# Performance work log

Measured on AMD Instinct MI355X. Metric: run time of the kernel, lower is better.

Reference implementation:

```python
import jax, jax.numpy as jnp
import numpy as np

B, S, HID, NH, AH, F = 1024, 100, 128, 2, 64, 2
DH = HID // NH          # item/pos head size = 64
DA = AH // NH           # attribute head size = 32
EPS = 1e-12


def setup_inputs() -> dict:
    key = jax.random.key(0)
    ks = iter(jax.random.split(key, 32))
    n = lambda shape, s=0.02: jax.random.normal(next(ks), shape, dtype=jnp.float32) * s
    inp = {
        "input_tensor": jax.random.normal(next(ks), (B, S, HID), dtype=jnp.float32),
        "attribute_table": jax.random.normal(next(ks), (F, B, S, AH), dtype=jnp.float32),
        "position_embedding": jax.random.normal(next(ks), (B, S, HID), dtype=jnp.float32),
        "attention_mask": jnp.zeros((B, 1, S, S), dtype=jnp.float32),
        # item / positional projections (stored [in, out])
        "Wq": n((HID, HID)), "bq": jnp.zeros((HID,), jnp.float32),
        "Wk": n((HID, HID)), "bk": jnp.zeros((HID,), jnp.float32),
        "Wv": n((HID, HID)), "bv": jnp.zeros((HID,), jnp.float32),
        "Wqp": n((HID, HID)), "bqp": jnp.zeros((HID,), jnp.float32),
        "Wkp": n((HID, HID)), "bkp": jnp.zeros((HID,), jnp.float32),
        # per-attribute projections, stacked over feat axis
        "Wq_attr": n((F, AH, AH)), "bq_attr": jnp.zeros((F, AH), jnp.float32),
        "Wk_attr": n((F, AH, AH)), "bk_attr": jnp.zeros((F, AH), jnp.float32),
        # gate fusion (VanillaAttentionX): Linear(S,S) -> ReLU -> Linear(S,1)
        "fuse_W1": n((S, S)), "fuse_b1": jnp.zeros((S,), jnp.float32),
        "fuse_W2": n((S, 1)), "fuse_b2": jnp.zeros((1,), jnp.float32),
        # output dense + LayerNorm
        "Wd": n((HID, HID)), "bd": jnp.zeros((HID,), jnp.float32),
        "ln_g": jnp.ones((HID,), jnp.float32), "ln_b": jnp.zeros((HID,), jnp.float32),
    }
    return inp


def _split_heads(x, nh):  # [B,S,nh*d] -> [B,nh,S,d]
    b, s, hd = x.shape
    return x.reshape(b, s, nh, hd // nh).transpose(0, 2, 1, 3)


def reference(input_tensor, attribute_table, position_embedding, attention_mask,
              Wq, bq, Wk, bk, Wv, bv, Wqp, bqp, Wkp, bkp,
              Wq_attr, bq_attr, Wk_attr, bk_attr,
              fuse_W1, fuse_b1, fuse_W2, fuse_b2,
              Wd, bd, ln_g, ln_b):
    b, s, hid = input_tensor.shape
    # item / positional QKV
    q = _split_heads(input_tensor @ Wq + bq, NH)
    k = _split_heads(input_tensor @ Wk + bk, NH)
    v = _split_heads(input_tensor @ Wv + bv, NH)
    qp = _split_heads(position_embedding @ Wqp + bqp, NH)
    kp = _split_heads(position_embedding @ Wkp + bkp, NH)
    item_scores = jnp.einsum('bhqd,bhkd->bhqk', q, k)
    pos_scores = jnp.einsum('bhqd,bhkd->bhqk', qp, kp)
    # attribute score streams: [F,B,S,AH] -> [F,B,NH,S,DA]
    aq = jnp.einsum('fbsa,fao->fbso', attribute_table, Wq_attr) + bq_attr[:, None, None, :]
    ak = jnp.einsum('fbsa,fao->fbso', attribute_table, Wk_attr) + bk_attr[:, None, None, :]
    aq = aq.reshape(F, b, s, NH, DA).transpose(0, 1, 3, 2, 4)
    ak = ak.reshape(F, b, s, NH, DA).transpose(0, 1, 3, 2, 4)
    attr_scores = jnp.einsum('fbhqd,fbhkd->fbhqk', aq, ak)  # [F,B,NH,S,S]
    # gate fusion: stack streams on axis -2 -> [B,NH,S,F+2,S]
    stacked = jnp.concatenate([
        jnp.moveaxis(attr_scores, 0, 3),
        item_scores[:, :, :, None, :],
        pos_scores[:, :, :, None, :],
    ], axis=-2)
    energy = jax.nn.relu(stacked @ fuse_W1 + fuse_b1) @ fuse_W2 + fuse_b2  # [B,NH,S,F+2,1]
    gate_w = jax.nn.softmax(energy[..., 0], axis=-1)                       # [B,NH,S,F+2]
    fused = jnp.einsum('bhsfk,bhsf->bhsk', stacked, gate_w)                # [B,NH,S,S]
    scores = fused / jnp.sqrt(jnp.asarray(DH, fused.dtype)) + attention_mask
    probs = jax.nn.softmax(scores, axis=-1)
    ctx = jnp.einsum('bhqk,bhkd->bhqd', probs, v)
    ctx = ctx.transpose(0, 2, 1, 3).reshape(b, s, hid)
    h = ctx @ Wd + bd + input_tensor
    mu = jnp.mean(h, axis=-1, keepdims=True)
    var = jnp.mean((h - mu) ** 2, axis=-1, keepdims=True)
    return (h - mu) / jnp.sqrt(var + EPS) * ln_g + ln_b
```

## Files before the change

### kernel.cpp

```cpp
#include <hip/hip_runtime.h>
#include <hip/hip_bf16.h>

using bf16 = __hip_bfloat16;
using u16 = unsigned short;
typedef __attribute__((ext_vector_type(8))) short bf16x8;
typedef __attribute__((ext_vector_type(16))) float f32x16;

namespace {

constexpr int B_  = 1024;
constexpr int Sd  = 100;
constexpr int BS_ = B_ * Sd;

constexpr int NTHR = 1024;
constexpr int NW   = 16;

constexpr int STP = 420;
constexpr int STS = 104;
constexpr int QKP = 196;
constexpr int AP  = 132;
constexpr int ATP = 68;
constexpr int W1P = 116;
constexpr int VTP = 116;

constexpr int O_ST = 0;
constexpr int O_Q  = 84000;
constexpr int O_K  = 123200;
constexpr int E2S  = 32000;
constexpr int LBYTES = 162400;

constexpr int WQT_E  = 0;
constexpr int WKT_E  = 16384;
constexpr int WQPT_E = 32768;
constexpr int WKPT_E = 49152;
constexpr int WVT_E  = 65536;
constexpr int WAT_E  = 81920;
constexpr int W1T_E  = 98304;
constexpr int WDT_E  = 113152;
constexpr size_t WS_NEED = 129536ull * 2;

__device__ __forceinline__ float bfr(u16 u) {
  unsigned int x = ((unsigned int)u) << 16;
  float f; __builtin_memcpy(&f, &x, 4); return f;
}
__device__ __forceinline__ u16 f2bu(float x) {
  bf16 h = __float2bfloat16(x);
  u16 u; __builtin_memcpy(&u, &h, 2); return u;
}
__device__ __forceinline__ float4 ld4(const float* p) {
  return *reinterpret_cast<const float4*>(p);
}
__device__ __forceinline__ float wsum(float v) {
#pragma unroll
  for (int m = 32; m > 0; m >>= 1) v += __shfl_xor(v, m);
  return v;
}
__device__ __forceinline__ float wmax(float v) {
#pragma unroll
  for (int m = 32; m > 0; m >>= 1) v = fmaxf(v, __shfl_xor(v, m));
  return v;
}
__device__ __forceinline__ f32x16 zf16() {
  f32x16 z;
#pragma unroll
  for (int i = 0; i < 16; ++i) z[i] = 0.f;
  return z;
}
__device__ __forceinline__ f32x16 MFMA32(bf16x8 a, bf16x8 b, f32x16 c) {
  return __builtin_amdgcn_mfma_f32_32x32x16_bf16(a, b, c, 0, 0, 0);
}

__device__ __forceinline__ bf16x8 ld8(const u16* p) {
  const ushort4 a = *reinterpret_cast<const ushort4*>(p);
  const ushort4 b = *reinterpret_cast<const ushort4*>(p + 4);
  bf16x8 f;
  f[0] = (short)a.x; f[1] = (short)a.y; f[2] = (short)a.z; f[3] = (short)a.w;
  f[4] = (short)b.x; f[5] = (short)b.y; f[6] = (short)b.z; f[7] = (short)b.w;
  return f;
}

template <int L4>
__device__ __forceinline__ void stage_rows4(const float* __restrict__ src, u16* dst,
                                            int nrow, int pitch, int tid, int nthr) {
  for (int i = tid; i < (nrow << L4); i += nthr) {
    const int rr = i >> L4, cc = (i & ((1 << L4) - 1)) << 2;
    const float4 v = *reinterpret_cast<const float4*>(src + ((size_t)rr << (L4 + 2)) + cc);
    ushort4 o;
    o.x = f2bu(v.x); o.y = f2bu(v.y); o.z = f2bu(v.z); o.w = f2bu(v.w);
    *reinterpret_cast<ushort4*>(dst + rr * pitch + cc) = o;
  }
}
template <int LC>
__device__ __forceinline__ void stage_wt(const float* __restrict__ W, int ldw, int coff,
                                         u16* dst, int kd, int pitch, int tid, int nthr) {
  constexpr int NC = 1 << LC;
  for (int idx = tid; idx < NC * kd; idx += nthr) {
    const int k = idx >> LC, c = idx & (NC - 1);
    dst[c * pitch + k] = f2bu(W[k * ldw + coff + c]);
  }
}
__device__ __forceinline__ void stage_wt6(const float* __restrict__ W, int coff,
                                          u16* dst, int tid, int nthr) {
  stage_wt<6>(W, 128, coff, dst, 128, AP, tid, nthr);
}
__device__ __forceinline__ void copy_w64(const u16* __restrict__ src, u16* dst,
                                         int tid, int nthr) {
  for (int i = tid; i < 2048; i += nthr) {
    const int r = i >> 5, c4 = (i & 31) << 2;
    *reinterpret_cast<ushort4*>(dst + r * AP + c4) =
        *reinterpret_cast<const ushort4*>(src + r * 128 + c4);
  }
}

template <int KD, bool TR>
__device__ __forceinline__ void tile32(const u16* A, int apitch, const u16* Wt, int wpitch,
                                       const float* __restrict__ bias, u16* dst, int dpitch,
                                       int dbase, int m0, int n0, int l) {
  const int cr = l & 31, g = l >> 5;
  int ar = m0 + cr; if (ar >= Sd) ar = Sd - 1;
  const u16* ap = A + ar * apitch + g * 8;
  const u16* bp = Wt + (n0 + cr) * wpitch + g * 8;
  f32x16 acc = zf16();
#pragma unroll
  for (int k0 = 0; k0 < KD; k0 += 16)
    acc = MFMA32(ld8(ap + k0), ld8(bp + k0), acc);
  const float bvv = bias[n0 + cr];
#pragma unroll
  for (int i = 0; i < 16; ++i) {
    const int row = m0 + (i & 3) + 8 * (i >> 2) + 4 * g;
    if (row < Sd) {
      if (TR) dst[(n0 + cr) * dpitch + dbase + row] = f2bu(acc[i] + bvv);
      else    dst[row * dpitch + dbase + n0 + cr]   = f2bu(acc[i] + bvv);
    }
  }
}

__global__ __launch_bounds__(256) void prep_weights(
    const float* __restrict__ Wq, const float* __restrict__ Wk,
    const float* __restrict__ Wqp, const float* __restrict__ Wkp,
    const float* __restrict__ Wv, const float* __restrict__ Wqa,
    const float* __restrict__ Wka, const float* __restrict__ W1,
    const float* __restrict__ Wd, u16* __restrict__ ws) {
  const int t = blockIdx.x * 256 + threadIdx.x;
  const int NT = gridDim.x * 256;
  const float* srcs[5] = {Wq, Wk, Wqp, Wkp, Wv};
#pragma unroll
  for (int wsel = 0; wsel < 5; ++wsel) {
    u16* dst = ws + wsel * 16384;
    const float* src = srcs[wsel];
    for (int i = t; i < 16384; i += NT) {
      const int h = i >> 13, c = (i >> 7) & 63, k = i & 127;
      dst[i] = f2bu(src[k * 128 + h * 64 + c]);
    }
  }
  for (int i = t; i < 16384; i += NT) {
    const int pr = i >> 12, h = (i >> 11) & 1, c = (i >> 6) & 31, k = i & 63;
    const float* src = (pr & 1) ? Wka : Wqa;
    ws[WAT_E + i] = f2bu(src[(pr >> 1) * 4096 + k * 64 + h * 32 + c]);
  }
  for (int i = t; i < 14848; i += NT) {
    const int c = i / W1P, k = i - c * W1P;
    ws[W1T_E + i] = (c < Sd && k < Sd) ? f2bu(W1[k * Sd + c]) : (u16)0;
  }
  for (int i = t; i < 16384; i += NT) {
    const int c = i >> 7, k = i & 127;
    ws[WDT_E + i] = f2bu(Wd[k * 128 + c]);
  }
}

template <bool PREP>
__global__ __launch_bounds__(NTHR) void attn_mega(
    const float* __restrict__ input, const float* __restrict__ attrT,
    const float* __restrict__ posE, const float* __restrict__ mask,
    const float* __restrict__ Wq, const float* __restrict__ bq,
    const float* __restrict__ Wk, const float* __restrict__ bk,
    const float* __restrict__ Wv, const float* __restrict__ bv,
    const float* __restrict__ Wqp, const float* __restrict__ bqp,
    const float* __restrict__ Wkp, const float* __restrict__ bkp,
    const float* __restrict__ Wqa, const float* __restrict__ bqa,
    const float* __restrict__ Wka, const float* __restrict__ bka,
    const float* __restrict__ W1, const float* __restrict__ b1,
    const float* __restrict__ W2, const u16* __restrict__ wsw,
    float* __restrict__ ctx) {
  __shared__ __align__(16) char L[LBYTES];
  u16* const ST = (u16*)(L + O_ST);
  u16* const QC = (u16*)(L + O_Q);
  u16* const KC = (u16*)(L + O_K);
  u16* const SA  = (u16*)(L + O_ST);
  u16* const SW1 = (u16*)(L + O_ST + 26400);
  u16* const SW2 = (u16*)(L + O_ST + 43296);
  u16* const AT0  = (u16*)(L + O_ST);
  u16* const AT1  = (u16*)(L + O_ST + 13600);
  u16* const WA0Q = (u16*)(L + O_ST + 27200);
  u16* const WA0K = (u16*)(L + O_ST + 31552);
  u16* const WA1Q = (u16*)(L + O_ST + 35904);
  u16* const WA1K = (u16*)(L + O_ST + 40256);
  u16* const W1T = (u16*)(L + O_K);
  float* const e2s = (float*)(L + O_K + E2S);
  u16* const VA  = (u16*)(L + O_Q);
  u16* const WVT = (u16*)(L + O_K);
  u16* const VT  = (u16*)(L + O_K + 16896);

  const int tid = threadIdx.x;
  const int bh = blockIdx.x;
  const int b = bh >> 1, h = bh & 1;
  const size_t row0 = (size_t)b * Sd;
  const int l = tid & 63, w = tid >> 6;
  const int cr = l & 31, g = l >> 5;

  stage_rows4<5>(input + row0 * 128, SA, 100, AP, tid, NTHR);
  if constexpr (PREP) {
    copy_w64(wsw + WQT_E + h * 8192, SW1, tid, NTHR);
    copy_w64(wsw + WKT_E + h * 8192, SW2, tid, NTHR);
  } else {
    stage_wt6(Wq, h * 64, SW1, tid, NTHR);
    stage_wt6(Wk, h * 64, SW2, tid, NTHR);
  }
  float4 r2[8];
#pragma unroll
  for (int s = 0; s < 8; ++s) {
    if (PREP && s >= 4) break;
    const int fi = tid + s * NTHR;
    if (fi < 3200) {
      r2[s] = ld4(posE + row0 * 128 + fi * 4);
    } else if (!PREP && fi < 5248) {
      const int f2 = fi - 3200, k = f2 >> 4, c0 = (f2 & 15) << 2;
      r2[s] = ld4(Wqp + k * 128 + h * 64 + c0);
    } else if (!PREP && fi < 7296) {
      const int f2 = fi - 5248, k = f2 >> 4, c0 = (f2 & 15) << 2;
      r2[s] = ld4(Wkp + k * 128 + h * 64 + c0);
    }
  }
  __syncthreads();

  {
    const int pr = w >> 3, mt = (w >> 1) & 3, nt = w & 1;
    tile32<128, false>(SA, AP, pr ? SW2 : SW1, AP, (pr ? bk : bq) + h * 64,
                       pr ? KC : QC, QKP, 0, mt * 32, nt * 32, l);
  }
  __syncthreads();

#pragma unroll
  for (int s = 0; s < 8; ++s) {
    if (PREP && s >= 4) break;
    const int fi = tid + s * NTHR;
    if (fi < 3200) {
      ushort4 o;
      o.x = f2bu(r2[s].x); o.y = f2bu(r2[s].y); o.z = f2bu(r2[s].z); o.w = f2bu(r2[s].w);
      *reinterpret_cast<ushort4*>(SA + (fi >> 5) * AP + ((fi & 31) << 2)) = o;
    } else if (!PREP && fi < 5248) {
      const int f2 = fi - 3200, k = f2 >> 4, c0 = (f2 & 15) << 2;
      SW1[c0 * AP + k] = f2bu(r2[s].x); SW1[(c0 + 1) * AP + k] = f2bu(r2[s].y);
      SW1[(c0 + 2) * AP + k] = f2bu(r2[s].z); SW1[(c0 + 3) * AP + k] = f2bu(r2[s].w);
    } else if (!PREP && fi < 7296) {
      const int f2 = fi - 5248, k = f2 >> 4, c0 = (f2 & 15) << 2;
      SW2[c0 * AP + k] = f2bu(r2[s].x); SW2[(c0 + 1) * AP + k] = f2bu(r2[s].y);
      SW2[(c0 + 2) * AP + k] = f2bu(r2[s].z); SW2[(c0 + 3) * AP + k] = f2bu(r2[s].w);
    }
  }
  if constexpr (PREP) {
    copy_w64(wsw + WQPT_E + h * 8192, SW1, tid, NTHR);
    copy_w64(wsw + WKPT_E + h * 8192, SW2, tid, NTHR);
  }
  float4 r3[6];
#pragma unroll
  for (int s = 0; s < 6; ++s) {
    if (PREP && s >= 4) break;
    const int fi = tid + s * NTHR;
    if (fi < 1600) {
      r3[s] = ld4(attrT + (size_t)b * 6400 + fi * 4);
    } else if (fi < 3200) {
      r3[s] = ld4(attrT + (size_t)(B_ + b) * 6400 + (fi - 1600) * 4);
    } else if (!PREP && fi < 5248) {
      const int f3 = fi - 3200, which = f3 >> 9, fj = f3 & 511;
      const int k = fj >> 3, c0 = (fj & 7) << 2;
      const float* src = (which == 0) ? Wqa : (which == 1) ? Wka
                       : (which == 2) ? (Wqa + 4096) : (Wka + 4096);
      r3[s] = ld4(src + k * 64 + h * 32 + c0);
    }
  }
  __syncthreads();

  {
    const int pr = w >> 3, mt = (w >> 1) & 3, nt = w & 1;
    tile32<128, false>(SA, AP, pr ? SW2 : SW1, AP, (pr ? bkp : bqp) + h * 64,
                       pr ? KC : QC, QKP, 64, mt * 32, nt * 32, l);
  }
  __syncthreads();

#pragma unroll
  for (int s = 0; s < 6; ++s) {
    if (PREP && s >= 4) break;
    const int fi = tid + s * NTHR;
    if (fi < 1600) {
      ushort4 o;
      o.x = f2bu(r3[s].x); o.y = f2bu(r3[s].y); o.z = f2bu(r3[s].z); o.w = f2bu(r3[s].w);
      *reinterpret_cast<ushort4*>(AT0 + (fi >> 4) * ATP + ((fi & 15) << 2)) = o;
    } else if (fi < 3200) {
      const int f3 = fi - 1600;
      ushort4 o;
      o.x = f2bu(r3[s].x); o.y = f2bu(r3[s].y); o.z = f2bu(r3[s].z); o.w = f2bu(r3[s].w);
      *reinterpret_cast<ushort4*>(AT1 + (f3 >> 4) * ATP + ((f3 & 15) << 2)) = o;
    } else if (!PREP && fi < 5248) {
      const int f3 = fi - 3200, which = f3 >> 9, fj = f3 & 511;
      const int k = fj >> 3, c0 = (fj & 7) << 2;
      u16* dst = (which == 0) ? WA0Q : (which == 1) ? WA0K
               : (which == 2) ? WA1Q : WA1K;
      dst[c0 * ATP + k] = f2bu(r3[s].x); dst[(c0 + 1) * ATP + k] = f2bu(r3[s].y);
      dst[(c0 + 2) * ATP + k] = f2bu(r3[s].z); dst[(c0 + 3) * ATP + k] = f2bu(r3[s].w);
    }
  }
  if constexpr (PREP) {
    for (int i = tid; i < 2048; i += NTHR) {
      const int pr = i >> 9, row = (i >> 4) & 31, c4 = (i & 15) << 2;
      u16* dst = (pr == 0) ? WA0Q : (pr == 1) ? WA0K : (pr == 2) ? WA1Q : WA1K;
      *reinterpret_cast<ushort4*>(dst + row * ATP + c4) =
          *reinterpret_cast<const ushort4*>(wsw + WAT_E + pr * 4096 + h * 2048 + row * 64 + c4);
    }
  }
  float4 r5[3];
  ushort4 rw1[4];
  if constexpr (PREP) {
#pragma unroll
    for (int s = 0; s < 4; ++s) {
      const int fi = tid + s * NTHR;
      if (fi < 3712) rw1[s] = reinterpret_cast<const ushort4*>(wsw + W1T_E)[fi];
    }
  } else {
#pragma unroll
    for (int s = 0; s < 3; ++s) {
      const int fi = tid + s * NTHR;
      if (fi < 2500) r5[s] = ld4(W1 + fi * 4);
    }
  }
  __syncthreads();

  {
    const int pr = w >> 2, mt = w & 3;
    const u16* Asrc = (pr < 2) ? AT0 : AT1;
    const u16* Wt = (pr == 0) ? WA0Q : (pr == 1) ? WA0K : (pr == 2) ? WA1Q : WA1K;
    const float* bs = (pr == 0) ? bqa + h * 32 : (pr == 1) ? bka + h * 32
                     : (pr == 2) ? bqa + 64 + h * 32 : bka + 64 + h * 32;
    tile32<64, false>(Asrc, ATP, Wt, ATP, bs, (pr & 1) ? KC : QC, QKP,
                      128 + (pr >> 1) * 32, mt * 32, 0, l);
  }
  __syncthreads();

  {
    ushort4 z; z.x = z.y = z.z = z.w = 0;
    for (int q = tid; q < Sd; q += NTHR)
      *reinterpret_cast<ushort4*>(ST + q * STP + 416) = z;
  }
  {
    const int mt = w >> 2, nt = w & 3;
    const int m0 = mt * 32, n0 = nt * 32;
    int ar = m0 + cr; if (ar >= Sd) ar = Sd - 1;
    int br = n0 + cr; if (br >= Sd) br = Sd - 1;
    const u16* ap = QC + ar * QKP + g * 8;
    const u16* bp = KC + br * QKP + g * 8;
    f32x16 ai = zf16(), po = zf16(), a0 = zf16(), a1 = zf16();
    ai = MFMA32(ld8(ap + 0),   ld8(bp + 0),   ai);
    ai = MFMA32(ld8(ap + 16),  ld8(bp + 16),  ai);
    ai = MFMA32(ld8(ap + 32),  ld8(bp + 32),  ai);
    ai = MFMA32(ld8(ap + 48),  ld8(bp + 48),  ai);
    po = MFMA32(ld8(ap + 64),  ld8(bp + 64),  po);
    po = MFMA32(ld8(ap + 80),  ld8(bp + 80),  po);
    po = MFMA32(ld8(ap + 96),  ld8(bp + 96),  po);
    po = MFMA32(ld8(ap + 112), ld8(bp + 112), po);
    a0 = MFMA32(ld8(ap + 128), ld8(bp + 128), a0);
    a0 = MFMA32(ld8(ap + 144), ld8(bp + 144), a0);
    a1 = MFMA32(ld8(ap + 160), ld8(bp + 160), a1);
    a1 = MFMA32(ld8(ap + 176), ld8(bp + 176), a1);
    const int col = n0 + cr;
    if (col < STS) {
#pragma unroll
      for (int i = 0; i < 16; ++i) {
        const int row = m0 + (i & 3) + 8 * (i >> 2) + 4 * g;
        if (row < Sd) {
          u16* sp = ST + row * STP + col;
          sp[0]       = f2bu(a0[i]);
          sp[STS]     = f2bu(a1[i]);
          sp[2 * STS] = f2bu(ai[i]);
          sp[3 * STS] = f2bu(po[i]);
        }
      }
    }
  }
  __syncthreads();

  if constexpr (PREP) {
#pragma unroll
    for (int s = 0; s < 4; ++s) {
      const int fi = tid + s * NTHR;
      if (fi < 3712) reinterpret_cast<ushort4*>(W1T)[fi] = rw1[s];
    }
  } else {
    {
      ushort4 z; z.x = z.y = z.z = z.w = 0;
      if (tid < 812)
        *reinterpret_cast<ushort4*>(W1T + 11600 + tid * 4) = z;
      if (tid < 400) {
        const int c = tid >> 2, kq = 100 + ((tid & 3) << 2);
        *reinterpret_cast<ushort4*>(W1T + c * W1P + kq) = z;
      }
    }
#pragma unroll
    for (int s = 0; s < 3; ++s) {
      const int fi = tid + s * NTHR;
      if (fi < 2500) {
#pragma unroll
        for (int j = 0; j < 4; ++j) {
          const int o = fi * 4 + j;
          const int k = o / 100, c = o - k * 100;
          W1T[c * W1P + k] = f2bu((j == 0) ? r5[s].x : (j == 1) ? r5[s].y
                                  : (j == 2) ? r5[s].z : r5[s].w);
        }
      }
    }
  }
  if (tid < 8) ((u16*)(L + O_Q))[tid] = 0;
  __syncthreads();

  {
    float b1v[4], w2v[4];
#pragma unroll
    for (int nt = 0; nt < 4; ++nt) {
      const int c = nt * 32 + cr;
      b1v[nt] = (c < Sd) ? b1[c] : 0.f;
      w2v[nt] = (c < Sd) ? W2[c] : 0.f;
    }
    for (int mt = w; mt < 13; mt += NW) {
      const int m0 = mt * 32;
      int gr = m0 + cr; if (gr > 399) gr = 399;
      const u16* ap = ST + (gr >> 2) * STP + (gr & 3) * STS + g * 8;
      f32x16 c0 = zf16(), c1 = zf16(), c2 = zf16(), c3 = zf16();
#pragma unroll
      for (int k0 = 0; k0 < 112; k0 += 16) {
        const bf16x8 af = ld8(ap + k0);
        c0 = MFMA32(af, ld8(W1T + (cr)      * W1P + g * 8 + k0), c0);
        c1 = MFMA32(af, ld8(W1T + (32 + cr) * W1P + g * 8 + k0), c1);
        c2 = MFMA32(af, ld8(W1T + (64 + cr) * W1P + g * 8 + k0), c2);
        c3 = MFMA32(af, ld8(W1T + (96 + cr) * W1P + g * 8 + k0), c3);
      }
#pragma unroll
      for (int i = 0; i < 16; ++i) {
        float v = fmaxf(c0[i] + b1v[0], 0.f) * w2v[0]
                + fmaxf(c1[i] + b1v[1], 0.f) * w2v[1]
                + fmaxf(c2[i] + b1v[2], 0.f) * w2v[2]
                + fmaxf(c3[i] + b1v[3], 0.f) * w2v[3];
#pragma unroll
        for (int mm = 1; mm < 32; mm <<= 1) v += __shfl_xor(v, mm);
        if (cr == 0) {
          const int go = m0 + (i & 3) + 8 * (i >> 2) + 4 * g;
          if (go < 400) e2s[go] = v;
        }
      }
    }
  }
  __syncthreads();

  {
    float4 va[4];
#pragma unroll
    for (int s = 0; s < 4; ++s) {
      const int fi = tid + s * NTHR;
      if (fi < 3200) va[s] = ld4(input + row0 * 128 + fi * 4);
    }
    ushort4 wv[2];
    if constexpr (PREP) {
#pragma unroll
      for (int s = 0; s < 2; ++s)
        wv[s] = reinterpret_cast<const ushort4*>(wsw + WVT_E + h * 8192)[tid + s * NTHR];
    }
    float m1r[7], m2r[7];
#pragma unroll
    for (int it = 0; it < 7; ++it) {
      const int q = w + it * NW;
      if (q < Sd) {
        const float* mp = mask + (size_t)b * 10000 + q * 100;
        m1r[it] = mp[l];
        m2r[it] = (l < 36) ? mp[64 + l] : 0.f;
      }
    }
    {
      ushort4 z; z.x = z.y = z.z = z.w = 0;
      for (int i2 = tid; i2 < 64 * VTP / 4; i2 += NTHR)
        *reinterpret_cast<ushort4*>(VT + i2 * 4) = z;
    }
#pragma unroll
    for (int it = 0; it < 7; ++it) {
      const int q = w + it * NW;
      if (q < Sd) {
        const float* ez = e2s + q * 4;
        float e0 = ez[0], e1 = ez[1], e2v = ez[2], e3 = ez[3];
        const float mg = fmaxf(fmaxf(e0, e1), fmaxf(e2v, e3));
        e0 = __expf(e0 - mg); e1 = __expf(e1 - mg);
        e2v = __expf(e2v - mg); e3 = __expf(e3 - mg);
        const float ginv = 1.0f / (e0 + e1 + e2v + e3);
        const float g0v = e0 * ginv, g1v = e1 * ginv, g2v = e2v * ginv, g3v = e3 * ginv;
        u16* const sp = ST + q * STP;
        float x1 = g0v * bfr(sp[l]) + g1v * bfr(sp[STS + l]) +
                   g2v * bfr(sp[2 * STS + l]) + g3v * bfr(sp[3 * STS + l]);
        x1 = x1 * 0.125f + m1r[it];
        const bool v2 = (l < 36);
        float x2 = -3e38f;
        if (v2) {
          const int k2 = 64 + l;
          x2 = g0v * bfr(sp[k2]) + g1v * bfr(sp[STS + k2]) +
               g2v * bfr(sp[2 * STS + k2]) + g3v * bfr(sp[3 * STS + k2]);
          x2 = x2 * 0.125f + m2r[it];
        }
        const float M = wmax(fmaxf(x1, x2));
        const float ea = __expf(x1 - M);
        const float eb = v2 ? __expf(x2 - M) : 0.f;
        const float inv = 1.0f / wsum(ea + eb);
        sp[l] = f2bu(ea * inv);
        if (v2) sp[64 + l] = f2bu(eb * inv);
      }
    }
#pragma unroll
    for (int s = 0; s < 4; ++s) {
      const int fi = tid + s * NTHR;
      if (fi < 3200) {
        ushort4 o;
        o.x = f2bu(va[s].x); o.y = f2bu(va[s].y); o.z = f2bu(va[s].z); o.w = f2bu(va[s].w);
        *reinterpret_cast<ushort4*>(VA + (fi >> 5) * AP + ((fi & 31) << 2)) = o;
      }
    }
    if constexpr (PREP) {
#pragma unroll
      for (int s = 0; s < 2; ++s) {
        const int i2 = tid + s * NTHR;
        const int r = i2 >> 5, c4 = (i2 & 31) << 2;
        *reinterpret_cast<ushort4*>(WVT + r * AP + c4) = wv[s];
      }
    } else {
      stage_wt6(Wv, h * 64, WVT, tid, NTHR);
    }
  }
  __syncthreads();

  if (w < 8) {
    const int mt = w >> 1, nt = w & 1;
    tile32<128, true>(VA, AP, WVT, AP, bv + h * 64, VT, VTP, 0, mt * 32, nt * 32, l);
  }
  __syncthreads();

  if (w < 8) {
    const int mt = w >> 1, nt = w & 1;
    const int m0 = mt * 32, n0 = nt * 32;
    int ar = m0 + cr; if (ar >= Sd) ar = Sd - 1;
    const u16* ap = ST + ar * STP + g * 8;
    const u16* bp = VT + (n0 + cr) * VTP + g * 8;
    f32x16 acc = zf16();
#pragma unroll
    for (int k0 = 0; k0 < 112; k0 += 16)
      acc = MFMA32(ld8(ap + k0), ld8(bp + k0), acc);
#pragma unroll
    for (int i = 0; i < 16; ++i) {
      const int row = m0 + (i & 3) + 8 * (i >> 2) + 4 * g;
      if (row < Sd)
        ctx[(row0 + row) * 128 + h * 64 + n0 + cr] = acc[i];
    }
  }
}

template <bool PREP>
__global__ __launch_bounds__(512) void dense_ln(
    const float* __restrict__ ctxg, const float* __restrict__ Wd,
    const float* __restrict__ bd, const float* __restrict__ resid,
    const float* __restrict__ lng, const float* __restrict__ lnb,
    const u16* __restrict__ wsw, float* __restrict__ out) {
  __shared__ __align__(16) char L[101376];
  u16* const Ab  = (u16*)L;
  u16* const WdT = (u16*)(L + 33792);
  u16* const Hs  = (u16*)(L + 67584);
  const int tid = threadIdx.x;
  const size_t row0 = (size_t)blockIdx.x * 128;
  const int l = tid & 63, w = tid >> 6, cr = l & 31, g = l >> 5;

  stage_rows4<5>(ctxg + row0 * 128, Ab, 128, AP, tid, 512);
  if constexpr (PREP) {
    for (int i = tid; i < 4096; i += 512) {
      const int r = i >> 5, c4 = (i & 31) << 2;
      *reinterpret_cast<ushort4*>(WdT + r * AP + c4) =
          *reinterpret_cast<const ushort4*>(wsw + WDT_E + r * 128 + c4);
    }
  } else {
    stage_wt<7>(Wd, 128, 0, WdT, 128, AP, tid, 512);
  }
  __syncthreads();

  for (int u = w; u < 16; u += 8) {
    const int m0 = (u >> 2) * 32, n0 = (u & 3) * 32;
    const u16* ap = Ab + (m0 + cr) * AP + g * 8;
    const u16* bp = WdT + (n0 + cr) * AP + g * 8;
    f32x16 acc = zf16();
#pragma unroll
    for (int k0 = 0; k0 < 128; k0 += 16)
      acc = MFMA32(ld8(ap + k0), ld8(bp + k0), acc);
#pragma unroll
    for (int i = 0; i < 16; ++i) {
      const int row = m0 + (i & 3) + 8 * (i >> 2) + 4 * g;
      Hs[row * AP + n0 + cr] = f2bu(acc[i]);
    }
  }
  __syncthreads();

  for (int rr = w; rr < 128; rr += 8) {
    const size_t grow = row0 + rr;
    const float h1 = bfr(Hs[rr * AP + l])      + bd[l]      + resid[grow * 128 + l];
    const float h2 = bfr(Hs[rr * AP + 64 + l]) + bd[64 + l] + resid[grow * 128 + 64 + l];
    const float mu = wsum(h1 + h2) * (1.0f / 128.0f);
    const float d1 = h1 - mu, d2 = h2 - mu;
    const float var = wsum(d1 * d1 + d2 * d2) * (1.0f / 128.0f);
    const float rs = rsqrtf(var + 1e-12f);
    out[grow * 128 + l]      = d1 * rs * lng[l]      + lnb[l];
    out[grow * 128 + 64 + l] = d2 * rs * lng[64 + l] + lnb[64 + l];
  }
}

}

extern "C" void kernel_launch(void* const* d_in, const int* in_sizes, int n_in,
                              void* d_out, int out_size, void* d_ws,
                              size_t ws_size, hipStream_t stream) {
  (void)in_sizes; (void)n_in; (void)out_size;

  const float* input = (const float*)d_in[0];
  const float* attrT = (const float*)d_in[1];
  const float* posE  = (const float*)d_in[2];
  const float* mask  = (const float*)d_in[3];
  const float* Wq  = (const float*)d_in[4];  const float* bq  = (const float*)d_in[5];
  const float* Wk  = (const float*)d_in[6];  const float* bk  = (const float*)d_in[7];
  const float* Wv  = (const float*)d_in[8];  const float* bv  = (const float*)d_in[9];
  const float* Wqp = (const float*)d_in[10]; const float* bqp = (const float*)d_in[11];
  const float* Wkp = (const float*)d_in[12]; const float* bkp = (const float*)d_in[13];
  const float* Wqa = (const float*)d_in[14]; const float* bqa = (const float*)d_in[15];
  const float* Wka = (const float*)d_in[16]; const float* bka = (const float*)d_in[17];
  const float* W1  = (const float*)d_in[18]; const float* b1  = (const float*)d_in[19];
  const float* W2  = (const float*)d_in[20];
  const float* Wd  = (const float*)d_in[22]; const float* bd  = (const float*)d_in[23];
  const float* lng = (const float*)d_in[24]; const float* lnb = (const float*)d_in[25];

  float* ctx = (float*)d_out;

  if (ws_size >= WS_NEED) {
    u16* wsw = (u16*)d_ws;
    prep_weights<<<dim3(128), dim3(256), 0, stream>>>(
        Wq, Wk, Wqp, Wkp, Wv, Wqa, Wka, W1, Wd, wsw);
    attn_mega<true><<<dim3(B_ * 2), dim3(NTHR), 0, stream>>>(
        input, attrT, posE, mask, Wq, bq, Wk, bk, Wv, bv, Wqp, bqp, Wkp, bkp,
        Wqa, bqa, Wka, bka, W1, b1, W2, wsw, ctx);
    dense_ln<true><<<dim3(BS_ / 128), dim3(512), 0, stream>>>(
        ctx, Wd, bd, input, lng, lnb, wsw, ctx);
  } else {
    attn_mega<false><<<dim3(B_ * 2), dim3(NTHR), 0, stream>>>(
        input, attrT, posE, mask, Wq, bq, Wk, bk, Wv, bv, Wqp, bqp, Wkp, bkp,
        Wqa, bqa, Wka, bka, W1, b1, W2, nullptr, ctx);
    dense_ln<false><<<dim3(BS_ / 128), dim3(512), 0, stream>>>(
        ctx, Wd, bd, input, lng, lnb, nullptr, ctx);
  }
}
```

Before: 318.3 us.

## Fuse LayerNorm into dense MFMA epilogue with register-resident rows and partial stats

The dense+LayerNorm kernel now keeps the MFMA accumulators in registers instead of writing bf16 results to shared memory and re-reading them row by row. Each wave computes two 32x32 tiles that share one B operand, adds bias and residual in the epilogue, and reduces per-row sum and sum-of-squares with shuffles. The partial stats go to a small shared buffer, which is combined after one barrier. This removes the Hs staging buffer and a bf16 rounding of h, and shrinks LDS. The trade-off is a single-pass variance (E[x^2]-mu^2, clamped at zero) that can lose precision, plus strided residual and output accesses in the MFMA layout.

```diff
diff --git a/kernel.cpp b/kernel.cpp
--- a/kernel.cpp
+++ b/kernel.cpp
@@ -571,10 +571,10 @@
     const float* __restrict__ bd, const float* __restrict__ resid,
     const float* __restrict__ lng, const float* __restrict__ lnb,
     const u16* __restrict__ wsw, float* __restrict__ out) {
-  __shared__ __align__(16) char L[101376];
-  u16* const Ab  = (u16*)L;
-  u16* const WdT = (u16*)(L + 33792);
-  u16* const Hs  = (u16*)(L + 67584);
+  __shared__ __align__(16) char L[71680];
+  u16* const Ab   = (u16*)L;
+  u16* const WdT  = (u16*)(L + 33792);
+  float* const rst = (float*)(L + 67584);
   const int tid = threadIdx.x;
   const size_t row0 = (size_t)blockIdx.x * 128;
   const int l = tid & 63, w = tid >> 6, cr = l & 31, g = l >> 5;
@@ -591,32 +591,67 @@
   }
   __syncthreads();
 
-  for (int u = w; u < 16; u += 8) {
-    const int m0 = (u >> 2) * 32, n0 = (u & 3) * 32;
-    const u16* ap = Ab + (m0 + cr) * AP + g * 8;
-    const u16* bp = WdT + (n0 + cr) * AP + g * 8;
-    f32x16 acc = zf16();
-#pragma unroll
-    for (int k0 = 0; k0 < 128; k0 += 16)
-      acc = MFMA32(ld8(ap + k0), ld8(bp + k0), acc);
-#pragma unroll
-    for (int i = 0; i < 16; ++i) {
-      const int row = m0 + (i & 3) + 8 * (i >> 2) + 4 * g;
-      Hs[row * AP + n0 + cr] = f2bu(acc[i]);
-    }
-  }
-  __syncthreads();
-
-  for (int rr = w; rr < 128; rr += 8) {
-    const size_t grow = row0 + rr;
-    const float h1 = bfr(Hs[rr * AP + l])      + bd[l]      + resid[grow * 128 + l];
-    const float h2 = bfr(Hs[rr * AP + 64 + l]) + bd[64 + l] + resid[grow * 128 + 64 + l];
-    const float mu = wsum(h1 + h2) * (1.0f / 128.0f);
-    const float d1 = h1 - mu, d2 = h2 - mu;
-    const float var = wsum(d1 * d1 + d2 * d2) * (1.0f / 128.0f);
-    const float rs = rsqrtf(var + 1e-12f);
-    out[grow * 128 + l]      = d1 * rs * lng[l]      + lnb[l];
-    out[grow * 128 + 64 + l] = d2 * rs * lng[64 + l] + lnb[64 + l];
+  const int nt = w & 3, col = nt * 32 + cr;
+  const int mA = (w >> 2) * 32, mB = mA + 64;
+  const float bdv = bd[col], lngv = lng[col], lnbv = lnb[col];
+
+  f32x16 hA = zf16(), hB = zf16();
+  {
+    const u16* bp  = WdT + col * AP + g * 8;
+    const u16* apA = Ab + (mA + cr) * AP + g * 8;
+    const u16* apB = Ab + (mB + cr) * AP + g * 8;
+#pragma unroll
+    for (int k0 = 0; k0 < 128; k0 += 16) {
+      const bf16x8 bf = ld8(bp + k0);
+      hA = MFMA32(ld8(apA + k0), bf, hA);
+      hB = MFMA32(ld8(apB + k0), bf, hB);
+    }
+  }
+
+#pragma unroll
+  for (int i = 0; i < 16; ++i) {
+    const int ro = (i & 3) + 8 * (i >> 2) + 4 * g;
+    const int rowA = mA + ro, rowB = mB + ro;
+    float a = hA[i] + bdv + resid[(row0 + rowA) * 128 + col];
+    float c = hB[i] + bdv + resid[(row0 + rowB) * 128 + col];
+    hA[i] = a; hB[i] = c;
+    float sA = a, qA = a * a, sB = c, qB = c * c;
+#pragma unroll
+    for (int m = 16; m > 0; m >>= 1) {
+      sA += __shfl_xor(sA, m); qA += __shfl_xor(qA, m);
+      sB += __shfl_xor(sB, m); qB += __shfl_xor(qB, m);
+    }
+    if (cr == 0) {
+      rst[rowA * 8 + nt * 2]     = sA;
+      rst[rowA * 8 + nt * 2 + 1] = qA;
+      rst[rowB * 8 + nt * 2]     = sB;
+      rst[rowB * 8 + nt * 2 + 1] = qB;
+    }
+  }
+  __syncthreads();
+
+#pragma unroll
+  for (int i = 0; i < 16; ++i) {
+    const int ro = (i & 3) + 8 * (i >> 2) + 4 * g;
+    const int rowA = mA + ro, rowB = mB + ro;
+    {
+      const float* p = rst + rowA * 8;
+      const float su = p[0] + p[2] + p[4] + p[6];
+      const float sq = p[1] + p[3] + p[5] + p[7];
+      const float mu = su * (1.0f / 128.0f);
+      const float var = fmaxf(sq * (1.0f / 128.0f) - mu * mu, 0.f);
+      const float rs = rsqrtf(var + 1e-12f);
+      out[(row0 + rowA) * 128 + col] = (hA[i] - mu) * rs * lngv + lnbv;
+    }
+    {
+      const float* p = rst + rowB * 8;
+      const float su = p[0] + p[2] + p[4] + p[6];
+      const float sq = p[1] + p[3] + p[5] + p[7];
+      const float mu = su * (1.0f / 128.0f);
+      const float var = fmaxf(sq * (1.0f / 128.0f) - mu * mu, 0.f);
+      const float rs = rsqrtf(var + 1e-12f);
+      out[(row0 + rowB) * 128 + col] = (hB[i] - mu) * rs * lngv + lnbv;
+    }
   }
 }
 
```

New measurement: 319.1 us. No clear change (+0.2%).
